# Kernel optimization log

Hardware: AMD Instinct MI355X
Metric: run time of the kernel (lower is better)

## Reference

```python
import jax, jax.numpy as jnp
import numpy as np

DIM = 768
HEADS = 12
DIM_HEAD = 64
INNER = HEADS * DIM_HEAD  # 768
SCALE = DIM_HEAD ** -0.5


def setup_inputs() -> dict:
    key = jax.random.key(0)
    k1, k2, k3, k4 = jax.random.split(key, 4)
    x = jax.random.normal(k1, (4, 1024, DIM), dtype=jnp.float32)
    # nn.Linear weights stored as [out, in]; we keep [in, out] for x @ W.
    w_qkv = jax.random.normal(k2, (DIM, 3 * INNER), dtype=jnp.float32) * (DIM ** -0.5)
    w_out = jax.random.normal(k3, (INNER, DIM), dtype=jnp.float32) * (INNER ** -0.5)
    b_out = jax.random.normal(k4, (DIM,), dtype=jnp.float32) * 0.02
    return {"x": x, "w_qkv": w_qkv, "w_out": w_out, "b_out": b_out}


def reference(x, w_qkv, w_out, b_out):
    B, N, _ = x.shape
    qkv = x @ w_qkv  # [B, N, 3*inner]
    q, k, v = jnp.split(qkv, 3, axis=-1)
    # b n (h d) -> b h n d
    def to_heads(t):
        return t.reshape(B, N, HEADS, DIM_HEAD).transpose(0, 2, 1, 3)
    q, k, v = to_heads(q), to_heads(k), to_heads(v)
    dots = jnp.einsum('bhnd,bhmd->bhnm', q, k) * SCALE  # [B, H, N, N]
    attn = jax.nn.softmax(dots, axis=-1)  # dropout p=0 -> identity
    out = jnp.einsum('bhnm,bhmd->bhnd', attn, v)
    out = out.transpose(0, 2, 1, 3).reshape(B, N, INNER)  # b h n d -> b n (h d)
    return out @ w_out + b_out
```

## Files before the change

kernel.cpp:

```cpp
#include <hip/hip_runtime.h>
#include <math.h>


typedef __attribute__((ext_vector_type(8))) __bf16 bf16x8;
typedef __attribute__((ext_vector_type(4))) float f32x4;
typedef __attribute__((ext_vector_type(16))) float f32x16;
typedef unsigned short u16;
typedef unsigned int u32;

#define ZERO16 {0,0,0,0,0,0,0,0,0,0,0,0,0,0,0,0}

__device__ __forceinline__ u16 f2bf(float f) {
    union { float f; unsigned u; } v; v.f = f;
    unsigned r = v.u + 0x7FFF + ((v.u >> 16) & 1);
    return (u16)(r >> 16);
}

__device__ __forceinline__ u32 cvtpk(float lo, float hi) {
    u32 r;
    asm("v_cvt_pk_bf16_f32 %0, %1, %2" : "=v"(r) : "v"(lo), "v"(hi));
    return r;
}
__device__ __forceinline__ float xhalf_max(float x) {
    float o = __shfl_xor(x, 32);
    return fmaxf(x, o);
}
__device__ __forceinline__ float xhalf_sum(float x) {
    float o = __shfl_xor(x, 32);
    return x + o;
}

__device__ __forceinline__ size_t fragoff(int m, int k) {
    return (((size_t)(m >> 4) * 24 + (k >> 5)) * 64 + (m & 15) + 16 * ((k & 31) >> 3)) * 8 + (k & 7);
}

__global__ __launch_bounds__(256) void prep(const float* __restrict__ x,
                                            const float* __restrict__ w_qkv,
                                            const float* __restrict__ w_out,
                                            u16* __restrict__ xA,
                                            u16* __restrict__ wB,
                                            u16* __restrict__ wO) {
    const int bid = blockIdx.x;
    const int tid = threadIdx.x;
    if (bid < 1536) {
        __shared__ float Tx[32][65];
        const int mt = bid & 127;
        const int kt = bid >> 7;
        const int r0 = mt * 32, k0 = kt * 64;
#pragma unroll
        for (int p = 0; p < 2; ++p) {
            int idx = tid + p * 256;
            int row = idx >> 4, c4 = idx & 15;
            float4 v = *reinterpret_cast<const float4*>(&x[(size_t)(r0 + row) * 768 + k0 + c4 * 4]);
            *reinterpret_cast<float4*>(&Tx[row][c4 * 4]) = v;
        }
        __syncthreads();
        const int f = tid >> 6, l = tid & 63;
        const int fm = f & 1, fk = f >> 1;
        const int lm = l & 15, lkc = l >> 4;
        const int lrow = fm * 16 + lm;
        const int lcol = fk * 32 + lkc * 8;
        float v0 = Tx[lrow][lcol + 0], v1 = Tx[lrow][lcol + 1];
        float v2 = Tx[lrow][lcol + 2], v3 = Tx[lrow][lcol + 3];
        float v4 = Tx[lrow][lcol + 4], v5 = Tx[lrow][lcol + 5];
        float v6 = Tx[lrow][lcol + 6], v7 = Tx[lrow][lcol + 7];
        int4 ov;
        ov.x = (int)cvtpk(v0, v1); ov.y = (int)cvtpk(v2, v3);
        ov.z = (int)cvtpk(v4, v5); ov.w = (int)cvtpk(v6, v7);
        *reinterpret_cast<int4*>(xA + fragoff(r0 + lrow, k0 + lcol)) = ov;
        return;
    }
    __shared__ float T[64][65];
    const float* in;
    u16* out;
    int C, n0, k0;
    if (bid < 1968) {
        int r = bid - 1536;
        in = w_qkv; out = wB; C = 2304;
        n0 = (r % 36) * 64; k0 = (r / 36) * 64;
    } else {
        int r = bid - 1968;
        in = w_out; out = wO; C = 768;
        n0 = (r % 12) * 64; k0 = (r / 12) * 64;
    }
#pragma unroll
    for (int p = 0; p < 16; ++p) {
        int idx = tid + p * 256;
        int row = idx >> 6, col = idx & 63;
        T[row][col] = in[(size_t)(k0 + row) * C + n0 + col];
    }
    __syncthreads();
#pragma unroll
    for (int q = 0; q < 2; ++q) {
        int lin = tid + q * 256;
        int nl = lin >> 3, kc = lin & 7;
        float v0 = T[kc * 8 + 0][nl], v1 = T[kc * 8 + 1][nl];
        float v2 = T[kc * 8 + 2][nl], v3 = T[kc * 8 + 3][nl];
        float v4 = T[kc * 8 + 4][nl], v5 = T[kc * 8 + 5][nl];
        float v6 = T[kc * 8 + 6][nl], v7 = T[kc * 8 + 7][nl];
        int4 ov;
        ov.x = (int)cvtpk(v0, v1); ov.y = (int)cvtpk(v2, v3);
        ov.z = (int)cvtpk(v4, v5); ov.w = (int)cvtpk(v6, v7);
        *reinterpret_cast<int4*>(out + fragoff(n0 + nl, k0 + kc * 8)) = ov;
    }
}

__global__ __launch_bounds__(256) void gemm_qkv(const u16* __restrict__ xA,
                                                const u16* __restrict__ wB,
                                                u16* __restrict__ Qf,
                                                u16* __restrict__ Kf,
                                                u16* __restrict__ Vf) {
    __shared__ u16 tile[4][64 * 68];
    const int tid = threadIdx.x;
    const int lane = tid & 63;
    const int w = tid >> 6;
    const int wm = w >> 1, wn = w & 1;
    const int lr = lane & 15;
    const int lk = lane >> 4;
    const int xcd = blockIdx.x & 7;
    const int lid = blockIdx.x >> 3;
    const int row0 = ((xcd & 3) * 8 + (lid & 7)) * 128;
    const int col0 = ((xcd >> 2) * 9 + (lid >> 3)) * 128;
    const int R0 = row0 + wm * 64;
    const int C0 = col0 + wn * 64;
    const u16* aB = xA + (size_t)(R0 >> 4) * 24 * 512 + lane * 8;
    const u16* bB = wB + (size_t)(C0 >> 4) * 24 * 512 + lane * 8;

    f32x4 acc[4][4];
#pragma unroll
    for (int mi = 0; mi < 4; ++mi)
#pragma unroll
        for (int nj = 0; nj < 4; ++nj) acc[mi][nj] = (f32x4){0.f, 0.f, 0.f, 0.f};

    int4 ra[3][4], rb[3][4];
#define LOADF(S, T)                                                           \
    {                                                                         \
        _Pragma("unroll")                                                     \
        for (int mi = 0; mi < 4; ++mi) {                                      \
            ra[S][mi] = *reinterpret_cast<const int4*>(aB + ((size_t)mi * 24 + (T)) * 512); \
            rb[S][mi] = *reinterpret_cast<const int4*>(bB + ((size_t)mi * 24 + (T)) * 512); \
        }                                                                     \
    }
#define COMPUTEF(S)                                                           \
    {                                                                         \
        union { int4 i; bf16x8 v; } af[4], bf[4];                             \
        _Pragma("unroll")                                                     \
        for (int mi = 0; mi < 4; ++mi) { af[mi].i = ra[S][mi]; bf[mi].i = rb[S][mi]; } \
        __builtin_amdgcn_s_setprio(1);                                        \
        _Pragma("unroll")                                                     \
        for (int mi = 0; mi < 4; ++mi)                                        \
            _Pragma("unroll")                                                 \
            for (int nj = 0; nj < 4; ++nj)                                    \
                acc[mi][nj] = __builtin_amdgcn_mfma_f32_16x16x32_bf16(af[mi].v, bf[nj].v, acc[mi][nj], 0, 0, 0); \
        __builtin_amdgcn_s_setprio(0);                                        \
    }

    LOADF(0, 0);
    LOADF(1, 1);
    LOADF(2, 2);
#pragma unroll
    for (int t = 0; t < 24; ++t) {
        COMPUTEF(t % 3);
        if (t + 3 < 24) { LOADF(t % 3, t + 3); }
    }
#undef LOADF
#undef COMPUTEF

    const int which = col0 / 768;
    const int cb = col0 - which * 768;
    const int c0w = cb + wn * 64;
    const int b = R0 >> 10;
    const int n0 = R0 & 1023;
    const int h = c0w >> 6;
    const int bh = b * 12 + h;
    u16* tw = &tile[w][0];

    if (which != 2) {
        const float qs = (which == 0) ? 0.18033688f : 1.0f;
#pragma unroll
        for (int mi = 0; mi < 4; ++mi)
#pragma unroll
            for (int i = 0; i < 4; ++i)
#pragma unroll
                for (int nj = 0; nj < 4; ++nj)
                    tw[(mi * 16 + lk * 4 + i) * 68 + nj * 16 + lr] = f2bf(acc[mi][nj][i] * qs);
        u16* dst = (which == 0) ? Qf : Kf;
#pragma unroll
        for (int fb = 0; fb < 2; ++fb)
#pragma unroll
            for (int kt2 = 0; kt2 < 4; ++kt2) {
                int4 v = *reinterpret_cast<const int4*>(
                    &tw[(fb * 32 + (lane & 31)) * 68 + kt2 * 16 + (lane >> 5) * 8]);
                size_t off = ((((size_t)bh * 32 + (n0 >> 5) + fb) * 4 + kt2) * 2) * 256 + (size_t)lane * 8;
                *reinterpret_cast<int4*>(dst + off) = v;
            }
    } else {
#pragma unroll
        for (int mi = 0; mi < 4; ++mi)
#pragma unroll
            for (int i = 0; i < 4; ++i)
#pragma unroll
                for (int nj = 0; nj < 4; ++nj)
                    tw[(nj * 16 + lr) * 68 + mi * 16 + lk * 4 + i] = f2bf(acc[mi][nj][i]);
#pragma unroll
        for (int ks = 0; ks < 4; ++ks)
#pragma unroll
            for (int hia = 0; hia < 2; ++hia) {
                int4 v = *reinterpret_cast<const int4*>(&tw[lane * 68 + ks * 16 + hia * 8]);
                size_t off = ((((size_t)bh * 16 + (n0 >> 6)) * 4 + ks) * 2 + hia) * 512 + (size_t)lane * 8;
                *reinterpret_cast<int4*>(Vf + off) = v;
            }
    }
}

#define GETO(dt, r) ((dt) == 0 ? o0[r] : o1[r])

__global__ __launch_bounds__(256) void attn_mfma(const u16* __restrict__ Qf,
                                                 const u16* __restrict__ Kf,
                                                 const u16* __restrict__ Vf,
                                                 u16* __restrict__ attnF) {
    __shared__ float OtM[2][64][33];
    __shared__ float Lm[2][32], Ll[2][32];
    __shared__ u16 Os[2][32][72];

    const int tid = threadIdx.x;
    const int lane = tid & 63;
    const int w = tid >> 6;
    const int qsub = w & 1;
    const int half = w >> 1;
    const int l31 = lane & 31;
    const int hi = lane >> 5;

    const int bid = blockIdx.x;
    const int lin = (bid & 7) * 96 + (bid >> 3);
    const int qt = lin & 15;
    const int bh = lin >> 4;

    const u16* Qh = Qf + (size_t)bh * 65536;
    const u16* Kh = Kf + (size_t)bh * 65536;
    const u16* Vh = Vf + (size_t)bh * 65536;

    bf16x8 qf[4];
#pragma unroll
    for (int kt = 0; kt < 4; ++kt)
        qf[kt] = *reinterpret_cast<const bf16x8*>(
            Qh + (((size_t)(qt * 2 + qsub) * 4 + kt) * 2 + hi) * 256 + l31 * 8);

    f32x16 o0 = ZERO16, o1 = ZERO16;
    float m = -1e30f, l = 0.f;

    for (int it = 0; it < 8; ++it) {
        const int kb0 = it * 4 + half * 2;
        const int kvb = it * 2 + half;

        bf16x8 kf0[4], kf1[4];
#pragma unroll
        for (int kt = 0; kt < 4; ++kt) {
            kf0[kt] = *reinterpret_cast<const bf16x8*>(
                Kh + (((size_t)kb0 * 4 + kt) * 2 + hi) * 256 + l31 * 8);
            kf1[kt] = *reinterpret_cast<const bf16x8*>(
                Kh + (((size_t)(kb0 + 1) * 4 + kt) * 2 + hi) * 256 + l31 * 8);
        }
        bf16x8 vf0[4], vf1[4];
#pragma unroll
        for (int ks = 0; ks < 4; ++ks) {
            const u16* vb = Vh + (((size_t)kvb * 4 + ks) * 2 + hi) * 512;
            vf0[ks] = *reinterpret_cast<const bf16x8*>(vb + l31 * 8);
            vf1[ks] = *reinterpret_cast<const bf16x8*>(vb + (l31 + 32) * 8);
        }

        f32x16 s0 = ZERO16, s1 = ZERO16;
        __builtin_amdgcn_s_setprio(1);
#pragma unroll
        for (int kt = 0; kt < 4; ++kt) s0 = __builtin_amdgcn_mfma_f32_32x32x16_bf16(kf0[kt], qf[kt], s0, 0, 0, 0);
#pragma unroll
        for (int kt = 0; kt < 4; ++kt) s1 = __builtin_amdgcn_mfma_f32_32x32x16_bf16(kf1[kt], qf[kt], s1, 0, 0, 0);
        __builtin_amdgcn_s_setprio(0);

        float mx[8];
#pragma unroll
        for (int i = 0; i < 8; ++i)
            mx[i] = fmaxf(fmaxf(s0[2*i], s0[2*i+1]), fmaxf(s1[2*i], s1[2*i+1]));
        float pmax = fmaxf(fmaxf(fmaxf(mx[0], mx[1]), fmaxf(mx[2], mx[3])),
                           fmaxf(fmaxf(mx[4], mx[5]), fmaxf(mx[6], mx[7])));
        pmax = xhalf_max(pmax);

        if (!__all(pmax <= m + 8.f)) {
            float mn = fmaxf(m, pmax);
            float c = __builtin_amdgcn_exp2f(m - mn);
            m = mn; l *= c;
            o0 = o0 * c; o1 = o1 * c;
        }

#pragma unroll
        for (int r = 0; r < 16; ++r) s0[r] = __builtin_amdgcn_exp2f(s0[r] - m);
#pragma unroll
        for (int r = 0; r < 16; ++r) s1[r] = __builtin_amdgcn_exp2f(s1[r] - m);
        float sm[8];
#pragma unroll
        for (int i = 0; i < 8; ++i)
            sm[i] = (s0[2*i] + s0[2*i+1]) + (s1[2*i] + s1[2*i+1]);
        float tsum = ((sm[0]+sm[1]) + (sm[2]+sm[3])) + ((sm[4]+sm[5]) + (sm[6]+sm[7]));
        l += xhalf_sum(tsum);

        bf16x8 pb[4];
#define PACK_GROUP(S, G, OUT)                                           \
        {                                                               \
            u32 X0 = cvtpk(S[8*(G)+0], S[8*(G)+1]);                     \
            u32 X1 = cvtpk(S[8*(G)+2], S[8*(G)+3]);                     \
            u32 Y0 = cvtpk(S[8*(G)+4], S[8*(G)+5]);                     \
            u32 Y1 = cvtpk(S[8*(G)+6], S[8*(G)+7]);                     \
            asm("v_permlane32_swap_b32 %0, %1" : "+v"(X0), "+v"(Y0));   \
            asm("v_permlane32_swap_b32 %0, %1" : "+v"(X1), "+v"(Y1));   \
            union { u32 u[4]; bf16x8 v; } pk_;                          \
            pk_.u[0] = X0;                                              \
            pk_.u[1] = X1;                                              \
            pk_.u[2] = Y0;                                              \
            pk_.u[3] = Y1;                                              \
            OUT = pk_.v;                                                \
        }
        PACK_GROUP(s0, 0, pb[0]);
        PACK_GROUP(s0, 1, pb[1]);
        PACK_GROUP(s1, 0, pb[2]);
        PACK_GROUP(s1, 1, pb[3]);
#undef PACK_GROUP

        __builtin_amdgcn_s_setprio(1);
#pragma unroll
        for (int ks = 0; ks < 4; ++ks) {
            o0 = __builtin_amdgcn_mfma_f32_32x32x16_bf16(vf0[ks], pb[ks], o0, 0, 0, 0);
            o1 = __builtin_amdgcn_mfma_f32_32x32x16_bf16(vf1[ks], pb[ks], o1, 0, 0, 0);
        }
        __builtin_amdgcn_s_setprio(0);
    }

    if (half == 1) {
#pragma unroll
        for (int dt = 0; dt < 2; ++dt)
#pragma unroll
            for (int r = 0; r < 16; ++r)
                OtM[qsub][dt * 32 + (r & 3) + 8 * (r >> 2) + 4 * hi][l31] = GETO(dt, r);
        Lm[qsub][l31] = m;
        Ll[qsub][l31] = l;
    }
    __syncthreads();
    if (half == 0) {
        float m2 = Lm[qsub][l31], l2 = Ll[qsub][l31];
        float mn = fmaxf(m, m2);
        float a = __builtin_amdgcn_exp2f(m - mn);
        float bsc = __builtin_amdgcn_exp2f(m2 - mn);
        float lm = l * a + l2 * bsc;
        float inv = 1.0f / lm;
        float av = a * inv, bv = bsc * inv;
#pragma unroll
        for (int dt = 0; dt < 2; ++dt)
#pragma unroll
            for (int rq = 0; rq < 4; ++rq) {
                int d0 = dt * 32 + 8 * rq + 4 * hi;
                float v0 = GETO(dt, rq * 4 + 0) * av + OtM[qsub][d0 + 0][l31] * bv;
                float v1 = GETO(dt, rq * 4 + 1) * av + OtM[qsub][d0 + 1][l31] * bv;
                float v2 = GETO(dt, rq * 4 + 2) * av + OtM[qsub][d0 + 2][l31] * bv;
                float v3 = GETO(dt, rq * 4 + 3) * av + OtM[qsub][d0 + 3][l31] * bv;
                uint2 pr;
                pr.x = cvtpk(v0, v1);
                pr.y = cvtpk(v2, v3);
                *reinterpret_cast<uint2*>(&Os[qsub][l31][d0]) = pr;
            }
    }
    __syncthreads();

    const int b = bh / 12, h = bh % 12;
    const int mbase = (b * 1024 + qt * 64) >> 4;
#pragma unroll
    for (int it2 = 0; it2 < 2; ++it2) {
        int idx = tid + it2 * 256;
        int f = idx >> 6;
        int l = idx & 63;
        int mt = f >> 1, kt2 = f & 1;
        int token = mt * 16 + (l & 15);
        int d = kt2 * 32 + (l >> 4) * 8;
        int4 v = *reinterpret_cast<const int4*>(&Os[token >> 5][token & 31][d]);
        size_t off = (((size_t)(mbase + mt) * 24 + (h * 2 + kt2)) * 64) * 8 + (size_t)l * 8;
        *reinterpret_cast<int4*>(attnF + off) = v;
    }
}

__global__ __launch_bounds__(256) void gemm_out(const u16* __restrict__ attnF,
                                                const u16* __restrict__ wO,
                                                const float* __restrict__ bias,
                                                float* __restrict__ out) {
    const int tid = threadIdx.x;
    const int lane = tid & 63;
    const int w = tid >> 6;
    const int wm = w >> 1, wn = w & 1;
    const int lr = lane & 15;
    const int lk = lane >> 4;
    const int xcd = blockIdx.x & 7;
    const int lid = blockIdx.x >> 3;
    const int row0 = (xcd * 4 + (lid & 3)) * 128;
    const int col0 = (lid >> 2) * 128;
    const int R0 = row0 + wm * 64;
    const int C0 = col0 + wn * 64;
    const u16* aB = attnF + (size_t)(R0 >> 4) * 24 * 512 + lane * 8;
    const u16* bB = wO + (size_t)(C0 >> 4) * 24 * 512 + lane * 8;

    f32x4 acc[4][4];
#pragma unroll
    for (int mi = 0; mi < 4; ++mi)
#pragma unroll
        for (int nj = 0; nj < 4; ++nj) acc[mi][nj] = (f32x4){0.f, 0.f, 0.f, 0.f};

    int4 ra[3][4], rb[3][4];
#define LOADF(S, T)                                                           \
    {                                                                         \
        _Pragma("unroll")                                                     \
        for (int mi = 0; mi < 4; ++mi) {                                      \
            ra[S][mi] = *reinterpret_cast<const int4*>(aB + ((size_t)mi * 24 + (T)) * 512); \
            rb[S][mi] = *reinterpret_cast<const int4*>(bB + ((size_t)mi * 24 + (T)) * 512); \
        }                                                                     \
    }
#define COMPUTEF(S)                                                           \
    {                                                                         \
        union { int4 i; bf16x8 v; } af[4], bf[4];                             \
        _Pragma("unroll")                                                     \
        for (int mi = 0; mi < 4; ++mi) { af[mi].i = ra[S][mi]; bf[mi].i = rb[S][mi]; } \
        __builtin_amdgcn_s_setprio(1);                                        \
        _Pragma("unroll")                                                     \
        for (int mi = 0; mi < 4; ++mi)                                        \
            _Pragma("unroll")                                                 \
            for (int nj = 0; nj < 4; ++nj)                                    \
                acc[mi][nj] = __builtin_amdgcn_mfma_f32_16x16x32_bf16(af[mi].v, bf[nj].v, acc[mi][nj], 0, 0, 0); \
        __builtin_amdgcn_s_setprio(0);                                        \
    }

    LOADF(0, 0);
    LOADF(1, 1);
    LOADF(2, 2);
#pragma unroll
    for (int t = 0; t < 24; ++t) {
        COMPUTEF(t % 3);
        if (t + 3 < 24) { LOADF(t % 3, t + 3); }
    }
#undef LOADF
#undef COMPUTEF

#pragma unroll
    for (int mi = 0; mi < 4; ++mi)
#pragma unroll
        for (int i = 0; i < 4; ++i) {
            int r = row0 + wm * 64 + mi * 16 + lk * 4 + i;
#pragma unroll
            for (int nj = 0; nj < 4; ++nj) {
                int c = col0 + wn * 64 + nj * 16 + lr;
                out[(size_t)r * 768 + c] = acc[mi][nj][i] + bias[c];
            }
        }
}

extern "C" void kernel_launch(void* const* d_in, const int* in_sizes, int n_in,
                              void* d_out, int out_size, void* d_ws, size_t ws_size,
                              hipStream_t stream) {
    const float* x     = (const float*)d_in[0];
    const float* w_qkv = (const float*)d_in[1];
    const float* w_out = (const float*)d_in[2];
    const float* b_out = (const float*)d_in[3];
    float* out = (float*)d_out;

    u16* ws = (u16*)d_ws;
    const size_t n_x = (size_t)4096 * 768;
    u16* xA     = ws;
    u16* wB     = xA + n_x;
    u16* wO     = wB + (size_t)2304 * 768;
    u16* Qfr    = wO + (size_t)768 * 768;
    u16* Kfr    = Qfr + n_x;
    u16* Vfr    = Kfr + n_x;
    u16* attnF  = Vfr + n_x;

    prep<<<2112, 256, 0, stream>>>(x, w_qkv, w_out, xA, wB, wO);
    gemm_qkv<<<576, 256, 0, stream>>>(xA, wB, Qfr, Kfr, Vfr);
    attn_mfma<<<768, 256, 0, stream>>>(Qfr, Kfr, Vfr, attnF);
    gemm_out<<<192, 256, 0, stream>>>(attnF, wO, b_out, out);
}
```

Measured before the change: 70.69 us.

## Split attention KV loop four ways per 32-query tile with tree merge

Each block now handles 32 queries instead of 64, and its four waves each take a quarter of the key/value sequence rather than two waves splitting it in half. The partial softmax states are combined through shared memory in a two-level merge, and the grid doubles to 1536 blocks. The aim is more parallelism and shorter per-wave serial loops, giving better CU occupancy and latency hiding. The cost is extra merge steps and barriers, and K/V are read twice as often across blocks because each block covers fewer queries.

```diff
diff --git a/kernel.cpp b/kernel.cpp
--- a/kernel.cpp
+++ b/kernel.cpp
@@ -221,20 +221,18 @@
                                                  u16* __restrict__ attnF) {
     __shared__ float OtM[2][64][33];
     __shared__ float Lm[2][32], Ll[2][32];
-    __shared__ u16 Os[2][32][72];
+    __shared__ u16 Os[32][72];
 
     const int tid = threadIdx.x;
     const int lane = tid & 63;
     const int w = tid >> 6;
-    const int qsub = w & 1;
-    const int half = w >> 1;
     const int l31 = lane & 31;
     const int hi = lane >> 5;
 
     const int bid = blockIdx.x;
-    const int lin = (bid & 7) * 96 + (bid >> 3);
-    const int qt = lin & 15;
-    const int bh = lin >> 4;
+    const int lin = (bid & 7) * 192 + (bid >> 3);
+    const int qt2 = lin & 31;
+    const int bh = lin >> 5;
 
     const u16* Qh = Qf + (size_t)bh * 65536;
     const u16* Kh = Kf + (size_t)bh * 65536;
@@ -244,14 +242,14 @@
 #pragma unroll
     for (int kt = 0; kt < 4; ++kt)
         qf[kt] = *reinterpret_cast<const bf16x8*>(
-            Qh + (((size_t)(qt * 2 + qsub) * 4 + kt) * 2 + hi) * 256 + l31 * 8);
+            Qh + (((size_t)qt2 * 4 + kt) * 2 + hi) * 256 + l31 * 8);
 
     f32x16 o0 = ZERO16, o1 = ZERO16;
     float m = -1e30f, l = 0.f;
 
-    for (int it = 0; it < 8; ++it) {
-        const int kb0 = it * 4 + half * 2;
-        const int kvb = it * 2 + half;
+    for (int it = 0; it < 4; ++it) {
+        const int kb0 = it * 8 + w * 2;
+        const int kvb = it * 4 + w;
 
         bf16x8 kf0[4], kf1[4];
 #pragma unroll
@@ -334,53 +332,72 @@
         __builtin_amdgcn_s_setprio(0);
     }
 
-    if (half == 1) {
-#pragma unroll
-        for (int dt = 0; dt < 2; ++dt)
-#pragma unroll
-            for (int r = 0; r < 16; ++r)
-                OtM[qsub][dt * 32 + (r & 3) + 8 * (r >> 2) + 4 * hi][l31] = GETO(dt, r);
-        Lm[qsub][l31] = m;
-        Ll[qsub][l31] = l;
-    }
+#define PUBLISH(SLOT)                                                         \
+    {                                                                         \
+        _Pragma("unroll")                                                     \
+        for (int dt = 0; dt < 2; ++dt)                                        \
+            _Pragma("unroll")                                                 \
+            for (int r = 0; r < 16; ++r)                                      \
+                OtM[SLOT][dt * 32 + (r & 3) + 8 * (r >> 2) + 4 * hi][l31] = GETO(dt, r); \
+        Lm[SLOT][l31] = m;                                                    \
+        Ll[SLOT][l31] = l;                                                    \
+    }
+#define MERGEIN(SLOT)                                                         \
+    {                                                                         \
+        float m2 = Lm[SLOT][l31], l2 = Ll[SLOT][l31];                         \
+        float mn = fmaxf(m, m2);                                              \
+        float a = __builtin_amdgcn_exp2f(m - mn);                             \
+        float bsc = __builtin_amdgcn_exp2f(m2 - mn);                          \
+        _Pragma("unroll")                                                     \
+        for (int r = 0; r < 16; ++r) {                                        \
+            int d = (r & 3) + 8 * (r >> 2) + 4 * hi;                          \
+            o0[r] = o0[r] * a + OtM[SLOT][d][l31] * bsc;                      \
+            o1[r] = o1[r] * a + OtM[SLOT][32 + d][l31] * bsc;                 \
+        }                                                                     \
+        l = l * a + l2 * bsc;                                                 \
+        m = mn;                                                               \
+    }
+
+    if (w == 1) PUBLISH(0);
+    if (w == 3) PUBLISH(1);
     __syncthreads();
-    if (half == 0) {
-        float m2 = Lm[qsub][l31], l2 = Ll[qsub][l31];
-        float mn = fmaxf(m, m2);
-        float a = __builtin_amdgcn_exp2f(m - mn);
-        float bsc = __builtin_amdgcn_exp2f(m2 - mn);
-        float lm = l * a + l2 * bsc;
-        float inv = 1.0f / lm;
-        float av = a * inv, bv = bsc * inv;
+    if (w == 0) MERGEIN(0);
+    if (w == 2) MERGEIN(1);
+    __syncthreads();
+    if (w == 2) PUBLISH(1);
+    __syncthreads();
+    if (w == 0) {
+        MERGEIN(1);
+        float inv = 1.0f / l;
 #pragma unroll
         for (int dt = 0; dt < 2; ++dt)
 #pragma unroll
             for (int rq = 0; rq < 4; ++rq) {
                 int d0 = dt * 32 + 8 * rq + 4 * hi;
-                float v0 = GETO(dt, rq * 4 + 0) * av + OtM[qsub][d0 + 0][l31] * bv;
-                float v1 = GETO(dt, rq * 4 + 1) * av + OtM[qsub][d0 + 1][l31] * bv;
-                float v2 = GETO(dt, rq * 4 + 2) * av + OtM[qsub][d0 + 2][l31] * bv;
-                float v3 = GETO(dt, rq * 4 + 3) * av + OtM[qsub][d0 + 3][l31] * bv;
+                float v0 = GETO(dt, rq * 4 + 0) * inv;
+                float v1 = GETO(dt, rq * 4 + 1) * inv;
+                float v2 = GETO(dt, rq * 4 + 2) * inv;
+                float v3 = GETO(dt, rq * 4 + 3) * inv;
                 uint2 pr;
                 pr.x = cvtpk(v0, v1);
                 pr.y = cvtpk(v2, v3);
-                *reinterpret_cast<uint2*>(&Os[qsub][l31][d0]) = pr;
+                *reinterpret_cast<uint2*>(&Os[l31][d0]) = pr;
             }
     }
+#undef PUBLISH
+#undef MERGEIN
     __syncthreads();
 
     const int b = bh / 12, h = bh % 12;
-    const int mbase = (b * 1024 + qt * 64) >> 4;
-#pragma unroll
-    for (int it2 = 0; it2 < 2; ++it2) {
-        int idx = tid + it2 * 256;
-        int f = idx >> 6;
-        int l = idx & 63;
+    const int mbase = (b * 1024 + qt2 * 32) >> 4;
+    {
+        int f = tid >> 6;
+        int l_ = tid & 63;
         int mt = f >> 1, kt2 = f & 1;
-        int token = mt * 16 + (l & 15);
-        int d = kt2 * 32 + (l >> 4) * 8;
-        int4 v = *reinterpret_cast<const int4*>(&Os[token >> 5][token & 31][d]);
-        size_t off = (((size_t)(mbase + mt) * 24 + (h * 2 + kt2)) * 64) * 8 + (size_t)l * 8;
+        int token = mt * 16 + (l_ & 15);
+        int d = kt2 * 32 + (l_ >> 4) * 8;
+        int4 v = *reinterpret_cast<const int4*>(&Os[token][d]);
+        size_t off = (((size_t)(mbase + mt) * 24 + (h * 2 + kt2)) * 64) * 8 + (size_t)l_ * 8;
         *reinterpret_cast<int4*>(attnF + off) = v;
     }
 }
@@ -478,6 +495,6 @@
 
     prep<<<2112, 256, 0, stream>>>(x, w_qkv, w_out, xA, wB, wO);
     gemm_qkv<<<576, 256, 0, stream>>>(xA, wB, Qfr, Kfr, Vfr);
-    attn_mfma<<<768, 256, 0, stream>>>(Qfr, Kfr, Vfr, attnF);
+    attn_mfma<<<1536, 256, 0, stream>>>(Qfr, Kfr, Vfr, attnF);
     gemm_out<<<192, 256, 0, stream>>>(attnF, wO, b_out, out);
 }
```

Measured after the change: 74.44 us. 5.3% more time.
